# Kernel optimization log

Measured on AMD Instinct MI355X. Metric: run time of the kernel, lower is better.

## Reference

```python
import jax, jax.numpy as jnp
import numpy as np

HIDDEN = 2048
HEADS = 16
HEAD_DIM = HIDDEN // HEADS  # 128
NUM_LATENTS = 16
LN_EPS = 1e-5


def setup_inputs() -> dict:
    key = jax.random.key(0)
    ks = jax.random.split(key, 16)
    B, S, D = 8, 4096, HIDDEN
    glorot = lambda k, fi, fo: jax.random.uniform(k, (fi, fo), jnp.float32,
                                                  -np.sqrt(6.0 / (fi + fo)), np.sqrt(6.0 / (fi + fo)))
    return {
        "hidden_states": jax.random.normal(ks[0], (B, S, D), jnp.float32),
        "ln_g": jnp.ones((D,), jnp.float32),
        "ln_b": jnp.zeros((D,), jnp.float32),
        "latents": 0.02 * jax.random.normal(ks[1], (NUM_LATENTS, D), jnp.float32),
        # weights stored as [in, out] (transpose of torch Linear.weight)
        "w_lq": glorot(ks[2], D, D), "b_lq": jnp.zeros((D,), jnp.float32),
        "w_k": glorot(ks[3], D, D), "b_k": jnp.zeros((D,), jnp.float32),
        "w_v": glorot(ks[4], D, D), "b_v": jnp.zeros((D,), jnp.float32),
        "w_lv": glorot(ks[5], D, D), "b_lv": jnp.zeros((D,), jnp.float32),
        "w_out": glorot(ks[6], D, D), "b_out": jnp.zeros((D,), jnp.float32),
    }


def reference(hidden_states, ln_g, ln_b, latents, w_lq, b_lq, w_k, b_k,
              w_v, b_v, w_lv, b_lv, w_out, b_out):
    x = hidden_states
    B, S, D = x.shape
    H, hd, L = HEADS, HEAD_DIM, latents.shape[0]
    # pre-LayerNorm
    mu = jnp.mean(x, axis=-1, keepdims=True)
    var = jnp.var(x, axis=-1, keepdims=True)
    h = (x - mu) / jnp.sqrt(var + LN_EPS) * ln_g + ln_b
    # projections
    k = (h @ w_k + b_k).reshape(B, S, H, hd)          # keys   [B,S,H,hd]
    v = (h @ w_v + b_v).reshape(B, S, H, hd)          # values [B,S,H,hd]
    q = (latents @ w_lq + b_lq).reshape(L, H, hd)     # latent queries [L,H,hd]
    # latent cross-attention: scores [B,H,L,S]
    scores = jnp.einsum("lhd,bshd->bhls", q, k) / np.sqrt(hd).astype(x.dtype)
    probs = jax.nn.softmax(scores, axis=-1)           # dropout is identity at eval
    ctx = jnp.einsum("bhls,bshd->blhd", probs, v).reshape(B, L, D)
    lv = ctx @ w_lv + b_lv                            # [B,L,D]
    pooled = jnp.mean(lv, axis=1, keepdims=True)      # [B,1,D]
    out = pooled @ w_out + b_out                      # [B,1,D]
    return x + jnp.broadcast_to(out, (B, S, D))       # residual add
```

## Files before the change

kernel.cpp:

```cpp
#include <hip/hip_runtime.h>
#include <hip/hip_bf16.h>

#define BB 8
#define SS 4096
#define DD 2048
#define HH 16
#define HDIM 128
#define LL 16
#define JJ 256
#define ROWS (BB*SS)
#define LN_EPS 1e-5f

typedef __attribute__((ext_vector_type(8))) short short8;
typedef __attribute__((ext_vector_type(4))) float f32x4;

typedef __attribute__((address_space(1))) const unsigned int gu32;
typedef __attribute__((address_space(3))) unsigned int lu32;
__device__ __forceinline__ void async16(const void* g, void* l) {
  __builtin_amdgcn_global_load_lds((gu32*)g, (lu32*)l, 16, 0, 0);
}

__device__ __forceinline__ unsigned short f2bf(float f) {
  unsigned int u = __builtin_bit_cast(unsigned int, f);
  u += 0x7fffu + ((u >> 16) & 1u);
  return (unsigned short)(u >> 16);
}
__device__ __forceinline__ float bf2f(unsigned short u) {
  unsigned int v = ((unsigned int)u) << 16;
  return __builtin_bit_cast(float, v);
}

__global__ __launch_bounds__(256) void k_q_part(const float* latents, const float* w_lq, float* qpart) {
  int c  = blockIdx.x * 256 + threadIdx.x;
  int e0 = blockIdx.y * 64;
  float acc[16];
#pragma unroll
  for (int l = 0; l < 16; ++l) acc[l] = 0.f;
  for (int e = e0; e < e0 + 64; ++e) {
    float w = w_lq[(size_t)e * 2048 + c];
#pragma unroll
    for (int l = 0; l < 16; ++l) acc[l] += latents[l * 2048 + e] * w;
  }
#pragma unroll
  for (int l = 0; l < 16; ++l) qpart[((size_t)blockIdx.y * 16 + l) * 2048 + c] = acc[l];
}

__global__ __launch_bounds__(256) void k_reduce(const float* part, const float* bias, float* out, int R) {
  int c = blockIdx.x * 256 + threadIdx.x;
  int r = blockIdx.y;
  float s = bias[c];
  for (int p = 0; p < 32; ++p) s += part[((size_t)p * R + r) * 2048 + c];
  out[r * 2048 + c] = s;
}

__global__ __launch_bounds__(256) void k_lnT(const float* x, const float* ln_g, const float* ln_b,
                                             short* h) {
  int row = blockIdx.x;
  int t = threadIdx.x;
  const float4* xr = (const float4*)(x + (size_t)row * 2048);
  float4 v0 = xr[t * 2];
  float4 v1 = xr[t * 2 + 1];
  float s  = v0.x + v0.y + v0.z + v0.w + v1.x + v1.y + v1.z + v1.w;
  float s2 = v0.x*v0.x + v0.y*v0.y + v0.z*v0.z + v0.w*v0.w
           + v1.x*v1.x + v1.y*v1.y + v1.z*v1.z + v1.w*v1.w;
#pragma unroll
  for (int o = 32; o; o >>= 1) { s += __shfl_down(s, o); s2 += __shfl_down(s2, o); }
  __shared__ float red[8];
  int wid = t >> 6;
  if ((t & 63) == 0) { red[wid] = s; red[4 + wid] = s2; }
  __syncthreads();
  float ts  = red[0] + red[1] + red[2] + red[3];
  float ts2 = red[4] + red[5] + red[6] + red[7];
  float mu   = ts * (1.0f / 2048.0f);
  float var  = ts2 * (1.0f / 2048.0f) - mu * mu;
  float rstd = rsqrtf(var + LN_EPS);
  const float4* gp = (const float4*)ln_g;
  const float4* bp = (const float4*)ln_b;
  float4 g0 = gp[t * 2], g1 = gp[t * 2 + 1];
  float4 b0 = bp[t * 2], b1 = bp[t * 2 + 1];
  short8 o;
  o[0] = (short)f2bf((v0.x - mu) * rstd * g0.x + b0.x);
  o[1] = (short)f2bf((v0.y - mu) * rstd * g0.y + b0.y);
  o[2] = (short)f2bf((v0.z - mu) * rstd * g0.z + b0.z);
  o[3] = (short)f2bf((v0.w - mu) * rstd * g0.w + b0.w);
  o[4] = (short)f2bf((v1.x - mu) * rstd * g1.x + b1.x);
  o[5] = (short)f2bf((v1.y - mu) * rstd * g1.y + b1.y);
  o[6] = (short)f2bf((v1.z - mu) * rstd * g1.z + b1.z);
  o[7] = (short)f2bf((v1.w - mu) * rstd * g1.w + b1.w);
  ((short8*)(h + (size_t)row * 2048))[t] = o;
}

__global__ __launch_bounds__(256) void k_wq(const float* w_k, const float* q, short* wq_t) {
  int e = blockIdx.x;
  __shared__ float wrow[2048];
  for (int i = threadIdx.x; i < 512; i += 256)
    ((float4*)wrow)[i] = ((const float4*)(w_k + (size_t)e * 2048))[i];
  __syncthreads();
  int j = threadIdx.x;
  int h = j >> 4, l = j & 15;
  const float* qrow = q + l * 2048 + h * 128;
  const float* wr = wrow + h * 128;
  float acc = 0.f;
#pragma unroll 8
  for (int d = 0; d < 128; ++d) acc += wr[d] * qrow[d];
  wq_t[(size_t)j * 2048 + e] = (short)f2bf(acc * 0.08838834764831845f);
}

__global__ __launch_bounds__(256, 2) void k_scores(const short* h, const short* wq_t, float* scores) {
  int s0 = blockIdx.x * 64;
  int b  = blockIdx.y;
  __shared__ short lds[2 * 16384 + 2 * 4096];
  int t = threadIdx.x, lane = t & 63, w = t >> 6;
  f32x4 zero = {0.f, 0.f, 0.f, 0.f};
  f32x4 acc[4][4];
#pragma unroll
  for (int m = 0; m < 4; ++m)
#pragma unroll
    for (int n = 0; n < 4; ++n) acc[m][n] = zero;

  int jlo = w * 8 + (lane >> 3);
  int kcs = (lane & 7) ^ ((lane >> 3) & 7);
  const short* hbase = h + ((size_t)(b * 4096 + s0)) * 2048;
  int koff0 = (((lane >> 4)) ^ (lane & 7)) * 8;
  int koff1 = ((4 + (lane >> 4)) ^ (lane & 7)) * 8;

  int cur = 0;
  {
#pragma unroll
    for (int i = 0; i < 8; ++i)
      async16(wq_t + (size_t)(i * 32 + jlo) * 2048 + kcs * 8,
              lds + (size_t)(i * 256 + w * 64) * 8);
#pragma unroll
    for (int i = 0; i < 2; ++i)
      async16(hbase + (size_t)(i * 32 + jlo) * 2048 + kcs * 8,
              lds + 32768 + (size_t)(i * 256 + w * 64) * 8);
  }
  __syncthreads();

  for (int it = 0; it < 32; ++it) {
    if (it < 31) {
      int k0 = (it + 1) * 64;
      short* lA1 = lds + (cur ^ 1) * 16384;
      short* lB1 = lds + 32768 + (cur ^ 1) * 4096;
#pragma unroll
      for (int i = 0; i < 8; ++i)
        async16(wq_t + (size_t)(i * 32 + jlo) * 2048 + k0 + kcs * 8,
                lA1 + (size_t)(i * 256 + w * 64) * 8);
#pragma unroll
      for (int i = 0; i < 2; ++i)
        async16(hbase + (size_t)(i * 32 + jlo) * 2048 + k0 + kcs * 8,
                lB1 + (size_t)(i * 256 + w * 64) * 8);
    }
    const short* lA = lds + cur * 16384;
    const short* lB = lds + 32768 + cur * 4096;
#pragma unroll
    for (int kk = 0; kk < 2; ++kk) {
      int ko = kk ? koff1 : koff0;
      short8 afr[4];
#pragma unroll
      for (int m = 0; m < 4; ++m)
        afr[m] = *(const short8*)(lA + (w * 64 + m * 16 + (lane & 15)) * 64 + ko);
#pragma unroll
      for (int n = 0; n < 4; ++n) {
        short8 bfr = *(const short8*)(lB + (n * 16 + (lane & 15)) * 64 + ko);
#pragma unroll
        for (int m = 0; m < 4; ++m)
          acc[m][n] = __builtin_amdgcn_mfma_f32_16x16x32_bf16(afr[m], bfr, acc[m][n], 0, 0, 0);
      }
    }
    __syncthreads();
    cur ^= 1;
  }

  int r4 = (lane >> 4) * 4, cc = lane & 15;
#pragma unroll
  for (int m = 0; m < 4; ++m) {
    int j = w * 64 + m * 16 + r4;
#pragma unroll
    for (int n = 0; n < 4; ++n) {
      int s = s0 + n * 16 + cc;
      float* dst = scores + ((size_t)b * 256 + j) * 4096 + s;
#pragma unroll
      for (int i = 0; i < 4; ++i) dst[(size_t)i * 4096] = acc[m][n][i];
    }
  }
}

__global__ __launch_bounds__(256) void k_smax_a(const float* scores, float* msum) {
  int j = blockIdx.x, b = blockIdx.y;
  const float* row = scores + ((size_t)b * 256 + j) * 4096;
  float v[16];
  float mx = -1e30f;
#pragma unroll
  for (int i = 0; i < 16; ++i) { v[i] = row[threadIdx.x + 256 * i]; mx = fmaxf(mx, v[i]); }
#pragma unroll
  for (int o = 32; o; o >>= 1) mx = fmaxf(mx, __shfl_xor(mx, o));
  __shared__ float redm[4], reds[4];
  if ((threadIdx.x & 63) == 0) redm[threadIdx.x >> 6] = mx;
  __syncthreads();
  mx = fmaxf(fmaxf(redm[0], redm[1]), fmaxf(redm[2], redm[3]));
  float sum = 0.f;
#pragma unroll
  for (int i = 0; i < 16; ++i) sum += __expf(v[i] - mx);
#pragma unroll
  for (int o = 32; o; o >>= 1) sum += __shfl_xor(sum, o);
  if ((threadIdx.x & 63) == 0) reds[threadIdx.x >> 6] = sum;
  __syncthreads();
  if (threadIdx.x == 0) {
    sum = reds[0] + reds[1] + reds[2] + reds[3];
    msum[(b * 256 + j) * 2]     = mx;
    msum[(b * 256 + j) * 2 + 1] = 1.0f / (16.0f * sum);
  }
}

__global__ __launch_bounds__(256) void k_smax_b(const float* scores, const float* msum, float* pbar) {
  int b = blockIdx.y, sc = blockIdx.x;
  int t = threadIdx.x, lane = t & 63, jq = t >> 6;
  int s = sc * 64 + lane;
  const float* srow = scores + ((size_t)(b * 256 + jq * 64)) * 4096 + s;
  const float* ms = msum + (b * 256 + jq * 64) * 2;
  float acc[4] = {0.f, 0.f, 0.f, 0.f};
  for (int jj = 0; jj < 64; ++jj) {
    float m  = ms[jj * 2];
    float iv = ms[jj * 2 + 1];
    float v = __expf(srow[(size_t)jj * 4096] - m) * iv;
    acc[jj >> 4] += v;
  }
#pragma unroll
  for (int r = 0; r < 4; ++r)
    pbar[((size_t)b * 16 + jq * 4 + r) * 4096 + s] = acc[r];
}

__global__ __launch_bounds__(256) void k_tbar2(const short* h, const float* pbar, float* Tpart) {
  int ec = blockIdx.x;
  int sp = blockIdx.y;
  int b  = blockIdx.z;
  int t  = threadIdx.x;
  int e0 = ec * 1024 + t * 4;
  __shared__ float lp[16 * 256];
  {
    int hh = t >> 4, so = (t & 15) * 16;
    const float4* src = (const float4*)(pbar + ((size_t)b * 16 + hh) * 4096 + sp * 256 + so);
    float4* dst = (float4*)(lp + hh * 256 + so);
#pragma unroll
    for (int i = 0; i < 4; ++i) dst[i] = src[i];
  }
  __syncthreads();
  f32x4 acc[16];
#pragma unroll
  for (int hh = 0; hh < 16; ++hh) acc[hh] = (f32x4){0.f, 0.f, 0.f, 0.f};

  const short* hbase = h + ((size_t)(b * 4096 + sp * 256)) * 2048 + e0;
  for (int si = 0; si < 256; si += 4) {
    float hv[4][4];
#pragma unroll
    for (int r = 0; r < 4; ++r) {
      short4 hh4 = *(const short4*)(hbase + (size_t)(si + r) * 2048);
      hv[r][0] = bf2f((unsigned short)hh4.x);
      hv[r][1] = bf2f((unsigned short)hh4.y);
      hv[r][2] = bf2f((unsigned short)hh4.z);
      hv[r][3] = bf2f((unsigned short)hh4.w);
    }
#pragma unroll
    for (int hh = 0; hh < 16; ++hh) {
      float4 ph = *(const float4*)(lp + hh * 256 + si);
#pragma unroll
      for (int c = 0; c < 4; ++c)
        acc[hh][c] += ph.x * hv[0][c] + ph.y * hv[1][c] + ph.z * hv[2][c] + ph.w * hv[3][c];
    }
  }
#pragma unroll
  for (int hh = 0; hh < 16; ++hh)
    *(f32x4*)(Tpart + ((size_t)((sp * 8 + b) * 16 + hh)) * 2048 + e0) = acc[hh];
}

__global__ __launch_bounds__(256) void k_tred(const float* Tpart, float* Tbar) {
  int bh = blockIdx.x;
  for (int e = threadIdx.x; e < 2048; e += 256) {
    float s = 0.f;
#pragma unroll
    for (int p = 0; p < 16; ++p) s += Tpart[((size_t)p * 128 + bh) * 2048 + e];
    Tbar[(size_t)bh * 2048 + e] = s;
  }
}

__global__ __launch_bounds__(256) void k_cbar_part(const float* Tbar, const float* w_v, float* part) {
  int c  = blockIdx.x * 256 + threadIdx.x;
  int e0 = blockIdx.y * 64;
  int h  = c >> 7;
  float acc[8];
#pragma unroll
  for (int b = 0; b < 8; ++b) acc[b] = 0.f;
  for (int e = e0; e < e0 + 64; ++e) {
    float wv = w_v[(size_t)e * 2048 + c];
#pragma unroll
    for (int b = 0; b < 8; ++b) acc[b] += Tbar[((size_t)b * 16 + h) * 2048 + e] * wv;
  }
#pragma unroll
  for (int b = 0; b < 8; ++b) part[((size_t)blockIdx.y * 8 + b) * 2048 + c] = acc[b];
}

__global__ __launch_bounds__(256) void k_vecmat_part(const float* vin, const float* W, float* part) {
  int c  = blockIdx.x * 256 + threadIdx.x;
  int e0 = blockIdx.y * 64;
  float acc[8];
#pragma unroll
  for (int b = 0; b < 8; ++b) acc[b] = 0.f;
  for (int e = e0; e < e0 + 64; ++e) {
    float wv = W[(size_t)e * 2048 + c];
#pragma unroll
    for (int b = 0; b < 8; ++b) acc[b] += vin[b * 2048 + e] * wv;
  }
#pragma unroll
  for (int b = 0; b < 8; ++b) part[((size_t)blockIdx.y * 8 + b) * 2048 + c] = acc[b];
}

__global__ __launch_bounds__(256) void k_resid(const float* x, const float* outv, float* out) {
  size_t i4 = (size_t)blockIdx.x * 256 + threadIdx.x;
  size_t total4 = (size_t)ROWS * 512;
  size_t stride = (size_t)gridDim.x * 256;
  for (; i4 < total4; i4 += stride) {
    int b  = (int)(i4 >> 21);
    int c4 = (int)(i4 & 511);
    float4 xv = ((const float4*)x)[i4];
    float4 ov = ((const float4*)outv)[b * 512 + c4];
    float4 o;
    o.x = xv.x + ov.x; o.y = xv.y + ov.y;
    o.z = xv.z + ov.z; o.w = xv.w + ov.w;
    ((float4*)out)[i4] = o;
  }
}

extern "C" void kernel_launch(void* const* d_in, const int* in_sizes, int n_in,
                              void* d_out, int out_size, void* d_ws, size_t ws_size,
                              hipStream_t stream) {
  const float* x       = (const float*)d_in[0];
  const float* ln_g    = (const float*)d_in[1];
  const float* ln_b    = (const float*)d_in[2];
  const float* latents = (const float*)d_in[3];
  const float* w_lq    = (const float*)d_in[4];
  const float* b_lq    = (const float*)d_in[5];
  const float* w_k     = (const float*)d_in[6];
  const float* w_v     = (const float*)d_in[8];
  const float* b_v     = (const float*)d_in[9];
  const float* w_lv    = (const float*)d_in[10];
  const float* b_lv    = (const float*)d_in[11];
  const float* w_out   = (const float*)d_in[12];
  const float* b_out   = (const float*)d_in[13];

  char* base = (char*)d_out;
  float* scores = (float*)(base);
  short* h      = (short*)(base + 33554432);
  float* Tpart  = (float*)(base + 167772160);
  float* pbar   = (float*)(base + 184549376);
  float* msum   = (float*)(base + 186646528);
  float* q      = (float*)(base + 186662912);
  short* wq_t   = (short*)(base + 186793984);
  float* Tbar   = (float*)(base + 187842560);
  float* cbar   = (float*)(base + 188366848);
  float* pooled = (float*)(base + 188432384);
  float* part   = (float*)(base + 188497920);
  float* outv   = (float*)d_ws;
  float* out    = (float*)d_out;

  k_q_part     <<<dim3(8, 32), 256, 0, stream>>>(latents, w_lq, part);
  k_reduce     <<<dim3(8, 16), 256, 0, stream>>>(part, b_lq, q, 16);
  k_lnT        <<<32768, 256, 0, stream>>>(x, ln_g, ln_b, h);
  k_wq         <<<2048, 256, 0, stream>>>(w_k, q, wq_t);
  k_scores     <<<dim3(64, 8), 256, 0, stream>>>(h, wq_t, scores);
  k_smax_a     <<<dim3(256, 8), 256, 0, stream>>>(scores, msum);
  k_smax_b     <<<dim3(64, 8), 256, 0, stream>>>(scores, msum, pbar);
  k_tbar2      <<<dim3(2, 16, 8), 256, 0, stream>>>(h, pbar, Tpart);
  k_tred       <<<128, 256, 0, stream>>>(Tpart, Tbar);
  k_cbar_part  <<<dim3(8, 32), 256, 0, stream>>>(Tbar, w_v, part);
  k_reduce     <<<dim3(8, 8), 256, 0, stream>>>(part, b_v, cbar, 8);
  k_vecmat_part<<<dim3(8, 32), 256, 0, stream>>>(cbar, w_lv, part);
  k_reduce     <<<dim3(8, 8), 256, 0, stream>>>(part, b_lv, pooled, 8);
  k_vecmat_part<<<dim3(8, 32), 256, 0, stream>>>(pooled, w_out, part);
  k_reduce     <<<dim3(8, 8), 256, 0, stream>>>(part, b_out, outv, 8);
  k_resid      <<<2048, 256, 0, stream>>>(x, outv, out);
}
```

Before: 469.5 us.

## Retile scores GEMM over S, split j into grid, and double Tbar split

The scores GEMM now tiles 256 sequence rows by 64 query columns per block, with a third grid dimension over j blocks, instead of 64 rows by all 256 columns. This raises block count from 512 to 512 but changes reuse: h tiles are loaded 4 times across j blocks rather than once. It also replaces the full __syncthreads with explicit vmcnt waits and raw barriers so the prefetch of the next tile can stay in flight while computing. The Tbar kernel halves its sequence chunk to double the grid, with the reduction and workspace offsets adjusted to fit twice as many partials.

```diff
diff --git a/kernel.cpp b/kernel.cpp
--- a/kernel.cpp
+++ b/kernel.cpp
@@ -107,9 +107,10 @@
 }
 
 __global__ __launch_bounds__(256, 2) void k_scores(const short* h, const short* wq_t, float* scores) {
-  int s0 = blockIdx.x * 64;
-  int b  = blockIdx.y;
-  __shared__ short lds[2 * 16384 + 2 * 4096];
+  int s0 = blockIdx.x * 256;
+  int j0 = blockIdx.y * 64;
+  int b  = blockIdx.z;
+  __shared__ short lds[2 * 4096 + 2 * 16384];
   int t = threadIdx.x, lane = t & 63, w = t >> 6;
   f32x4 zero = {0.f, 0.f, 0.f, 0.f};
   f32x4 acc[4][4];
@@ -118,67 +119,74 @@
 #pragma unroll
     for (int n = 0; n < 4; ++n) acc[m][n] = zero;
 
-  int jlo = w * 8 + (lane >> 3);
-  int kcs = (lane & 7) ^ ((lane >> 3) & 7);
-  const short* hbase = h + ((size_t)(b * 4096 + s0)) * 2048;
+  int rsel = t >> 3;
+  int kcs  = (t & 7) ^ ((t >> 3) & 7);
+  const short* hbase  = h + ((size_t)(b * 4096 + s0)) * 2048;
+  const short* wqbase = wq_t + (size_t)j0 * 2048;
   int koff0 = (((lane >> 4)) ^ (lane & 7)) * 8;
   int koff1 = ((4 + (lane >> 4)) ^ (lane & 7)) * 8;
 
   int cur = 0;
   {
+    short* lA = lds;
+    short* lB = lds + 8192;
 #pragma unroll
     for (int i = 0; i < 8; ++i)
-      async16(wq_t + (size_t)(i * 32 + jlo) * 2048 + kcs * 8,
-              lds + (size_t)(i * 256 + w * 64) * 8);
+      async16(hbase + (size_t)(i * 32 + rsel) * 2048 + kcs * 8,
+              lB + (i * 256 + w * 64) * 8);
 #pragma unroll
     for (int i = 0; i < 2; ++i)
-      async16(hbase + (size_t)(i * 32 + jlo) * 2048 + kcs * 8,
-              lds + 32768 + (size_t)(i * 256 + w * 64) * 8);
-  }
-  __syncthreads();
+      async16(wqbase + (size_t)(i * 32 + rsel) * 2048 + kcs * 8,
+              lA + (i * 256 + w * 64) * 8);
+  }
 
   for (int it = 0; it < 32; ++it) {
     if (it < 31) {
       int k0 = (it + 1) * 64;
-      short* lA1 = lds + (cur ^ 1) * 16384;
-      short* lB1 = lds + 32768 + (cur ^ 1) * 4096;
+      short* lA1 = lds + (cur ^ 1) * 4096;
+      short* lB1 = lds + 8192 + (cur ^ 1) * 16384;
 #pragma unroll
       for (int i = 0; i < 8; ++i)
-        async16(wq_t + (size_t)(i * 32 + jlo) * 2048 + k0 + kcs * 8,
-                lA1 + (size_t)(i * 256 + w * 64) * 8);
+        async16(hbase + (size_t)(i * 32 + rsel) * 2048 + k0 + kcs * 8,
+                lB1 + (i * 256 + w * 64) * 8);
 #pragma unroll
       for (int i = 0; i < 2; ++i)
-        async16(hbase + (size_t)(i * 32 + jlo) * 2048 + k0 + kcs * 8,
-                lB1 + (size_t)(i * 256 + w * 64) * 8);
-    }
-    const short* lA = lds + cur * 16384;
-    const short* lB = lds + 32768 + cur * 4096;
+        async16(wqbase + (size_t)(i * 32 + rsel) * 2048 + k0 + kcs * 8,
+                lA1 + (i * 256 + w * 64) * 8);
+      asm volatile("s_waitcnt vmcnt(10)" ::: "memory");
+    } else {
+      asm volatile("s_waitcnt vmcnt(0)" ::: "memory");
+    }
+    __builtin_amdgcn_s_barrier();
+    __builtin_amdgcn_sched_barrier(0);
+    const short* lA = lds + cur * 4096;
+    const short* lB = lds + 8192 + cur * 16384;
 #pragma unroll
     for (int kk = 0; kk < 2; ++kk) {
       int ko = kk ? koff1 : koff0;
       short8 afr[4];
 #pragma unroll
       for (int m = 0; m < 4; ++m)
-        afr[m] = *(const short8*)(lA + (w * 64 + m * 16 + (lane & 15)) * 64 + ko);
+        afr[m] = *(const short8*)(lA + (m * 16 + (lane & 15)) * 64 + ko);
 #pragma unroll
       for (int n = 0; n < 4; ++n) {
-        short8 bfr = *(const short8*)(lB + (n * 16 + (lane & 15)) * 64 + ko);
+        short8 bfr = *(const short8*)(lB + (w * 64 + n * 16 + (lane & 15)) * 64 + ko);
 #pragma unroll
         for (int m = 0; m < 4; ++m)
           acc[m][n] = __builtin_amdgcn_mfma_f32_16x16x32_bf16(afr[m], bfr, acc[m][n], 0, 0, 0);
       }
     }
-    __syncthreads();
+    __builtin_amdgcn_s_barrier();
     cur ^= 1;
   }
 
   int r4 = (lane >> 4) * 4, cc = lane & 15;
 #pragma unroll
   for (int m = 0; m < 4; ++m) {
-    int j = w * 64 + m * 16 + r4;
+    int j = j0 + m * 16 + r4;
 #pragma unroll
     for (int n = 0; n < 4; ++n) {
-      int s = s0 + n * 16 + cc;
+      int s = s0 + w * 64 + n * 16 + cc;
       float* dst = scores + ((size_t)b * 256 + j) * 4096 + s;
 #pragma unroll
       for (int i = 0; i < 4; ++i) dst[(size_t)i * 4096] = acc[m][n][i];
@@ -237,21 +245,20 @@
   int b  = blockIdx.z;
   int t  = threadIdx.x;
   int e0 = ec * 1024 + t * 4;
-  __shared__ float lp[16 * 256];
+  __shared__ float lp[16 * 128];
   {
-    int hh = t >> 4, so = (t & 15) * 16;
-    const float4* src = (const float4*)(pbar + ((size_t)b * 16 + hh) * 4096 + sp * 256 + so);
-    float4* dst = (float4*)(lp + hh * 256 + so);
-#pragma unroll
-    for (int i = 0; i < 4; ++i) dst[i] = src[i];
+    int hh = t >> 4, so = (t & 15) * 8;
+    const float4* src = (const float4*)(pbar + ((size_t)b * 16 + hh) * 4096 + sp * 128 + so);
+    float4* dst = (float4*)(lp + hh * 128 + so);
+    dst[0] = src[0]; dst[1] = src[1];
   }
   __syncthreads();
   f32x4 acc[16];
 #pragma unroll
   for (int hh = 0; hh < 16; ++hh) acc[hh] = (f32x4){0.f, 0.f, 0.f, 0.f};
 
-  const short* hbase = h + ((size_t)(b * 4096 + sp * 256)) * 2048 + e0;
-  for (int si = 0; si < 256; si += 4) {
+  const short* hbase = h + ((size_t)(b * 4096 + sp * 128)) * 2048 + e0;
+  for (int si = 0; si < 128; si += 4) {
     float hv[4][4];
 #pragma unroll
     for (int r = 0; r < 4; ++r) {
@@ -263,7 +270,7 @@
     }
 #pragma unroll
     for (int hh = 0; hh < 16; ++hh) {
-      float4 ph = *(const float4*)(lp + hh * 256 + si);
+      float4 ph = *(const float4*)(lp + hh * 128 + si);
 #pragma unroll
       for (int c = 0; c < 4; ++c)
         acc[hh][c] += ph.x * hv[0][c] + ph.y * hv[1][c] + ph.z * hv[2][c] + ph.w * hv[3][c];
@@ -279,7 +286,7 @@
   for (int e = threadIdx.x; e < 2048; e += 256) {
     float s = 0.f;
 #pragma unroll
-    for (int p = 0; p < 16; ++p) s += Tpart[((size_t)p * 128 + bh) * 2048 + e];
+    for (int p = 0; p < 32; ++p) s += Tpart[((size_t)p * 128 + bh) * 2048 + e];
     Tbar[(size_t)bh * 2048 + e] = s;
   }
 }
@@ -352,14 +359,14 @@
   float* scores = (float*)(base);
   short* h      = (short*)(base + 33554432);
   float* Tpart  = (float*)(base + 167772160);
-  float* pbar   = (float*)(base + 184549376);
-  float* msum   = (float*)(base + 186646528);
-  float* q      = (float*)(base + 186662912);
-  short* wq_t   = (short*)(base + 186793984);
-  float* Tbar   = (float*)(base + 187842560);
-  float* cbar   = (float*)(base + 188366848);
-  float* pooled = (float*)(base + 188432384);
-  float* part   = (float*)(base + 188497920);
+  float* pbar   = (float*)(base + 201326592);
+  float* msum   = (float*)(base + 203423744);
+  float* q      = (float*)(base + 203440128);
+  short* wq_t   = (short*)(base + 203571200);
+  float* Tbar   = (float*)(base + 204619776);
+  float* cbar   = (float*)(base + 205144064);
+  float* pooled = (float*)(base + 205209600);
+  float* part   = (float*)(base + 205275136);
   float* outv   = (float*)d_ws;
   float* out    = (float*)d_out;
 
@@ -367,10 +374,10 @@
   k_reduce     <<<dim3(8, 16), 256, 0, stream>>>(part, b_lq, q, 16);
   k_lnT        <<<32768, 256, 0, stream>>>(x, ln_g, ln_b, h);
   k_wq         <<<2048, 256, 0, stream>>>(w_k, q, wq_t);
-  k_scores     <<<dim3(64, 8), 256, 0, stream>>>(h, wq_t, scores);
+  k_scores     <<<dim3(16, 4, 8), 256, 0, stream>>>(h, wq_t, scores);
   k_smax_a     <<<dim3(256, 8), 256, 0, stream>>>(scores, msum);
   k_smax_b     <<<dim3(64, 8), 256, 0, stream>>>(scores, msum, pbar);
-  k_tbar2      <<<dim3(2, 16, 8), 256, 0, stream>>>(h, pbar, Tpart);
+  k_tbar2      <<<dim3(2, 32, 8), 256, 0, stream>>>(h, pbar, Tpart);
   k_tred       <<<128, 256, 0, stream>>>(Tpart, Tbar);
   k_cbar_part  <<<dim3(8, 32), 256, 0, stream>>>(Tbar, w_v, part);
   k_reduce     <<<dim3(8, 8), 256, 0, stream>>>(part, b_v, cbar, 8);
```

New measurement: 476.7 us. No clear change (+1.5%).
